# Kernel tuning notes

Hardware: AMD Instinct MI355X
Metric: run time of the kernel (lower is better)

The kernel has to match this reference:

```python
import jax, jax.numpy as jnp
import numpy as np

DIM = 384
HEADS = 6
K = 3  # kernel_size, stride = 1


def setup_inputs() -> dict:
    key = jax.random.key(0)
    ks = jax.random.split(key, 7)
    B, H, W, C = 16, 56, 56, DIM
    sc = 1.0 / np.sqrt(C)
    return {
        "x_map": jax.random.normal(ks[0], (B, H, W, C), dtype=jnp.float32),
        # Linear weights stored [in, out] (torch stores [out, in]; math identical)
        "W_attn": jax.random.normal(ks[1], (C, HEADS * K * K), dtype=jnp.float32) * sc,
        "b_attn": jax.random.normal(ks[2], (HEADS * K * K,), dtype=jnp.float32) * 0.02,
        "W_v": jax.random.normal(ks[3], (C, C), dtype=jnp.float32) * sc,
        "b_v": jax.random.normal(ks[4], (C,), dtype=jnp.float32) * 0.02,
        "W_proj": jax.random.normal(ks[5], (C, C), dtype=jnp.float32) * sc,
        "b_proj": jax.random.normal(ks[6], (C,), dtype=jnp.float32) * 0.02,
    }


def reference(x_map, W_attn, b_attn, W_v, b_v, W_proj, b_proj):
    B, H, W, C = x_map.shape
    k, heads = K, HEADS
    hd = C // heads
    pad = k // 2

    # attention logits per output pixel: [B, H*W, heads, k*k], softmax over window
    a = x_map @ W_attn + b_attn                     # [B,H,W,heads*k*k]
    a = jax.nn.softmax(a.reshape(B, H * W, heads, k * k), axis=-1)

    v = x_map @ W_v + b_v                           # [B,H,W,C]
    vp = jnp.pad(v, ((0, 0), (pad, pad), (pad, pad), (0, 0)))
    # k*k shifted views == F.unfold with row-major (ki,kj) kernel order
    patches = jnp.stack(
        [vp[:, i:i + H, j:j + W, :] for i in range(k) for j in range(k)],
        axis=3,
    )                                               # [B,H,W,k*k,C]
    patches = patches.reshape(B, H * W, k * k, heads, hd)

    # softmax-weighted sum over the k*k window, per head
    y = jnp.einsum('bpKhd,bphK->bphd', patches, a)  # [B,H*W,heads,hd]
    y = y.reshape(B, H, W, C)
    return y @ W_proj + b_proj
```

## Files before the change

kernel.cpp:

```cpp
#include <hip/hip_runtime.h>
#include <math.h>

#define NPIX 50176
#define CDIM 384
#define HEADS 6
#define NLOGIT 54
#define HH 56
#define WW 56
#define NCAT 448
#define KSTEPS 12
#define NCH_V 28
#define NCH_P 24

typedef __attribute__((ext_vector_type(8))) __bf16 bf16x8;
typedef __attribute__((ext_vector_type(4))) float f32x4;

__device__ __forceinline__ void glds16(const void* g, void* l) {
  __builtin_amdgcn_global_load_lds(
      (const __attribute__((address_space(1))) unsigned int*)g,
      (__attribute__((address_space(3))) unsigned int*)l, 16, 0, 0);
}

__global__ __launch_bounds__(256) void prep_kernel(
    const float* __restrict__ W_v, const float* __restrict__ W_proj,
    const float* __restrict__ W_attn, const float* __restrict__ b_attn,
    __bf16* __restrict__ Wcat_frag, __bf16* __restrict__ Wtp_frag,
    float* __restrict__ bpad) {
  const int gid = blockIdx.x * 256 + threadIdx.x;
  const int NV = KSTEPS * NCH_V * 64;
  const int NP = KSTEPS * NCH_P * 64;
  if (gid < NV) {
    const int ks   = gid / (NCH_V * 64);
    const int rem  = gid % (NCH_V * 64);
    const int ni   = rem >> 6;
    const int lane = rem & 63;
    const int n  = ni * 16 + (lane & 15);
    const int kb = ks * 32 + (lane >> 4) * 8;
    bf16x8 o;
    #pragma unroll
    for (int q = 0; q < 8; ++q) {
      const int k = kb + q;
      float val;
      if (n < CDIM) val = W_v[k * CDIM + n];
      else {
        const int nn = n - CDIM;
        val = (nn < NLOGIT) ? W_attn[k * NLOGIT + nn] : 0.f;
      }
      o[q] = (__bf16)val;
    }
    *(bf16x8*)&Wcat_frag[(size_t)gid * 8] = o;
  } else if (gid < NV + NP) {
    const int r    = gid - NV;
    const int ks   = r / (NCH_P * 64);
    const int rem  = r % (NCH_P * 64);
    const int ni   = rem >> 6;
    const int lane = rem & 63;
    const int n  = ni * 16 + (lane & 15);
    const int kb = ks * 32 + (lane >> 4) * 8;
    bf16x8 o;
    #pragma unroll
    for (int q = 0; q < 8; ++q) o[q] = (__bf16)W_proj[(kb + q) * CDIM + n];
    *(bf16x8*)&Wtp_frag[(size_t)r * 8] = o;
  } else if (gid < NV + NP + 64) {
    const int n = gid - NV - NP;
    bpad[n] = (n < NLOGIT) ? b_attn[n] : 0.f;
  }
}

__global__ __launch_bounds__(256) void gemm_v_logit_kernel(
    const float* __restrict__ X, const __bf16* __restrict__ Wcat_frag,
    const float* __restrict__ b_v, __bf16* __restrict__ v,
    const float* __restrict__ bpad, float* __restrict__ attn) {
  __shared__ char smem[NCH_V * 1024];
  __bf16* Bs = (__bf16*)smem;
  float (*Ls)[68] = (float(*)[68])smem;

  const int tid  = threadIdx.x;
  const int wave = tid >> 6;
  const int lane = tid & 63;
  const int bm   = blockIdx.x * 64;
  const int frow = lane & 15;
  const int fk8  = (lane >> 4) * 8;

  const int arow = bm + wave * 16 + frow;
  const float* xrow = X + (size_t)arow * CDIM + fk8;

  f32x4 acc[28] = {};
  float4 pa0 = *(const float4*)(xrow + 0);
  float4 pa1 = *(const float4*)(xrow + 4);

  for (int ks = 0; ks < KSTEPS; ++ks) {
    #pragma unroll
    for (int c = 0; c < 7; ++c) {
      const int chunk = wave * 7 + c;
      glds16(Wcat_frag + ((size_t)(ks * NCH_V + chunk) * 64 + lane) * 8,
             Bs + chunk * 512);
    }
    bf16x8 a;
    a[0] = (__bf16)pa0.x; a[1] = (__bf16)pa0.y; a[2] = (__bf16)pa0.z; a[3] = (__bf16)pa0.w;
    a[4] = (__bf16)pa1.x; a[5] = (__bf16)pa1.y; a[6] = (__bf16)pa1.z; a[7] = (__bf16)pa1.w;
    if (ks < KSTEPS - 1) {
      pa0 = *(const float4*)(xrow + (ks + 1) * 32 + 0);
      pa1 = *(const float4*)(xrow + (ks + 1) * 32 + 4);
    }
    __syncthreads();

    #pragma unroll
    for (int ni = 0; ni < 28; ++ni) {
      const bf16x8 b = *(const bf16x8*)&Bs[(ni * 64 + lane) * 8];
      acc[ni] = __builtin_amdgcn_mfma_f32_16x16x32_bf16(a, b, acc[ni], 0, 0, 0);
    }
    __syncthreads();
  }

  const int orow = (lane >> 4) * 4;

  #pragma unroll
  for (int ni = 0; ni < 24; ++ni) {
    const int n = ni * 16 + frow;
    const float bvl = b_v[n];
    #pragma unroll
    for (int r = 0; r < 4; ++r) {
      const int m = bm + wave * 16 + orow + r;
      v[(size_t)m * CDIM + n] = (__bf16)(acc[ni][r] + bvl);
    }
  }

  float bvl[4];
  #pragma unroll
  for (int ni = 0; ni < 4; ++ni) bvl[ni] = bpad[ni * 16 + frow];
  #pragma unroll
  for (int ni = 0; ni < 4; ++ni)
    #pragma unroll
    for (int r = 0; r < 4; ++r)
      Ls[wave * 16 + orow + r][ni * 16 + frow] = acc[24 + ni][r] + bvl[ni];
  __syncthreads();

  #pragma unroll
  for (int it = 0; it < 2; ++it) {
    const int task = it * 256 + tid;
    if (task < 64 * HEADS) {
      const int pl = task / HEADS;
      const int h  = task % HEADS;
      const float* row = &Ls[pl][h * 9];
      float m = row[0];
      #pragma unroll
      for (int w = 1; w < 9; ++w) m = fmaxf(m, row[w]);
      float e[9], s = 0.f;
      #pragma unroll
      for (int w = 0; w < 9; ++w) { e[w] = __expf(row[w] - m); s += e[w]; }
      const float inv = 1.f / s;
      float* op = &attn[(size_t)(bm + pl) * NLOGIT + h * 9];
      #pragma unroll
      for (int w = 0; w < 9; ++w) op[w] = e[w] * inv;
    }
  }
}

__global__ __launch_bounds__(256) void gemm_proj_kernel(
    const __bf16* __restrict__ Y, const __bf16* __restrict__ Wtp_frag,
    const float* __restrict__ bias, float* __restrict__ Out) {
  __shared__ __bf16 Bs[NCH_P * 512];

  const int tid  = threadIdx.x;
  const int wave = tid >> 6;
  const int lane = tid & 63;
  const int bm   = blockIdx.x * 64;
  const int frow = lane & 15;
  const int fk8  = (lane >> 4) * 8;

  const int arow = bm + wave * 16 + frow;
  const __bf16* yrow = Y + (size_t)arow * CDIM + fk8;

  f32x4 acc[24] = {};
  bf16x8 a = *(const bf16x8*)(yrow);

  for (int ks = 0; ks < KSTEPS; ++ks) {
    #pragma unroll
    for (int c = 0; c < 6; ++c) {
      const int chunk = wave * 6 + c;
      glds16(Wtp_frag + ((size_t)(ks * NCH_P + chunk) * 64 + lane) * 8,
             Bs + chunk * 512);
    }
    bf16x8 a_next;
    if (ks < KSTEPS - 1) a_next = *(const bf16x8*)(yrow + (ks + 1) * 32);
    __syncthreads();

    #pragma unroll
    for (int ni = 0; ni < 24; ++ni) {
      const bf16x8 b = *(const bf16x8*)&Bs[(ni * 64 + lane) * 8];
      acc[ni] = __builtin_amdgcn_mfma_f32_16x16x32_bf16(a, b, acc[ni], 0, 0, 0);
    }
    __syncthreads();
    a = a_next;
  }

  const int orow = (lane >> 4) * 4;
  #pragma unroll
  for (int ni = 0; ni < 24; ++ni) {
    const int n = ni * 16 + frow;
    const float bvl = bias[n];
    #pragma unroll
    for (int r = 0; r < 4; ++r) {
      const int m = bm + wave * 16 + orow + r;
      Out[(size_t)m * CDIM + n] = acc[ni][r] + bvl;
    }
  }
}

__global__ __launch_bounds__(256) void aggregate_kernel(
    const __bf16* __restrict__ v, const float* __restrict__ attn,
    __bf16* __restrict__ y) {
  const int idx = blockIdx.x * 256 + threadIdx.x;
  const int cg = idx % 48;
  const int pg = idx / 48;
  const int c  = cg * 8;
  const int b  = pg / ((HH / 4) * WW);
  const int r2 = pg % ((HH / 4) * WW);
  const int i0 = (r2 / WW) * 4;
  const int j  = r2 % WW;
  const int head = c >> 6;

  const int pbase = (b * HH + i0) * WW + j;
  float aw[4][9];
  #pragma unroll
  for (int p = 0; p < 4; ++p) {
    const float* ap = attn + (size_t)(pbase + p * WW) * NLOGIT + head * 9;
    #pragma unroll
    for (int w = 0; w < 9; ++w) aw[p][w] = ap[w];
  }

  const bool j0ok = (j > 0), j2ok = (j < WW - 1);
  float acc[4][8] = {};

  #pragma unroll
  for (int li = 0; li < 6; ++li) {
    const int ii = i0 - 1 + li;
    if (ii < 0 || ii >= HH) continue;
    const __bf16* vrow = v + ((size_t)(b * HH + ii) * WW + j) * CDIM + c;
    float ch[3][8];
    #pragma unroll
    for (int kj = 0; kj < 3; ++kj) {
      const bool ok = (kj == 0) ? j0ok : (kj == 2) ? j2ok : true;
      if (ok) {
        const bf16x8 vv = *(const bf16x8*)(vrow + (kj - 1) * CDIM);
        #pragma unroll
        for (int q = 0; q < 8; ++q) ch[kj][q] = (float)vv[q];
      } else {
        #pragma unroll
        for (int q = 0; q < 8; ++q) ch[kj][q] = 0.f;
      }
    }
    #pragma unroll
    for (int p = 0; p < 4; ++p) {
      const int ki = li - p;
      if (ki < 0 || ki > 2) continue;
      #pragma unroll
      for (int kj = 0; kj < 3; ++kj) {
        const float w = aw[p][ki * 3 + kj];
        #pragma unroll
        for (int q = 0; q < 8; ++q) acc[p][q] += w * ch[kj][q];
      }
    }
  }

  #pragma unroll
  for (int p = 0; p < 4; ++p) {
    bf16x8 o;
    #pragma unroll
    for (int q = 0; q < 8; ++q) o[q] = (__bf16)acc[p][q];
    *(bf16x8*)&y[(size_t)(pbase + p * WW) * CDIM + c] = o;
  }
}

extern "C" void kernel_launch(void* const* d_in, const int* in_sizes, int n_in,
                              void* d_out, int out_size, void* d_ws,
                              size_t ws_size, hipStream_t stream) {
  const float* x      = (const float*)d_in[0];
  const float* W_attn = (const float*)d_in[1];
  const float* b_attn = (const float*)d_in[2];
  const float* W_v    = (const float*)d_in[3];
  const float* b_v    = (const float*)d_in[4];
  const float* W_proj = (const float*)d_in[5];
  const float* b_proj = (const float*)d_in[6];
  float* out = (float*)d_out;

  char* w = (char*)d_ws;
  __bf16* v    = (__bf16*)w;  w += (size_t)NPIX * CDIM * 2;
  __bf16* y    = (__bf16*)w;  w += (size_t)NPIX * CDIM * 2;
  float*  attn = (float*)w;   w += (size_t)NPIX * NLOGIT * 4;
  __bf16* Wcat_frag = (__bf16*)w;  w += (size_t)NCAT * CDIM * 2;
  __bf16* Wtp_frag  = (__bf16*)w;  w += (size_t)CDIM * CDIM * 2;
  float*  bpad = (float*)w;   w += 64 * 4;

  const int prep_n = KSTEPS * NCH_V * 64 + KSTEPS * NCH_P * 64 + 64;
  prep_kernel<<<(prep_n + 255) / 256, 256, 0, stream>>>(
      W_v, W_proj, W_attn, b_attn, Wcat_frag, Wtp_frag, bpad);

  gemm_v_logit_kernel<<<NPIX / 64, 256, 0, stream>>>(
      x, Wcat_frag, b_v, v, bpad, attn);

  aggregate_kernel<<<(NPIX / 4 * 48) / 256, 256, 0, stream>>>(v, attn, y);

  gemm_proj_kernel<<<NPIX / 64, 256, 0, stream>>>(y, Wtp_frag, b_proj, out);
}
```

Measured before the change: 118.1 us.

## Split GEMM N dimension across two blocks and double-buffer weight tiles in LDS

Both GEMM kernels now launch a 2D grid that splits the output columns in half. Each block holds half the accumulators (14 or 12 fragments instead of 28 or 24), which lowers register pressure and doubles the block count. Weight tiles are double-buffered in LDS: the next K-step is prefetched while the current one runs, so one barrier per step replaces two. The cost is that each A row is now read and converted by both N-halves, doubling X traffic, and the softmax epilogue runs only in the by==1 blocks, which creates load imbalance.

```diff
diff --git a/kernel.cpp b/kernel.cpp
--- a/kernel.cpp
+++ b/kernel.cpp
@@ -71,88 +71,110 @@
     const float* __restrict__ X, const __bf16* __restrict__ Wcat_frag,
     const float* __restrict__ b_v, __bf16* __restrict__ v,
     const float* __restrict__ bpad, float* __restrict__ attn) {
-  __shared__ char smem[NCH_V * 1024];
-  __bf16* Bs = (__bf16*)smem;
+  __shared__ char smem[2 * 14 * 1024];
   float (*Ls)[68] = (float(*)[68])smem;
 
   const int tid  = threadIdx.x;
   const int wave = tid >> 6;
   const int lane = tid & 63;
   const int bm   = blockIdx.x * 64;
+  const int by   = blockIdx.y;
+  const int nbase = by * 14;
   const int frow = lane & 15;
   const int fk8  = (lane >> 4) * 8;
 
   const int arow = bm + wave * 16 + frow;
   const float* xrow = X + (size_t)arow * CDIM + fk8;
 
-  f32x4 acc[28] = {};
+  f32x4 acc[14] = {};
+
+  #pragma unroll
+  for (int c = 0; c < 4; ++c) {
+    const int chunk = wave * 4 + c;
+    if (chunk < 14)
+      glds16(Wcat_frag + ((size_t)(0 * NCH_V + nbase + chunk) * 64 + lane) * 8,
+             (__bf16*)smem + chunk * 512);
+  }
   float4 pa0 = *(const float4*)(xrow + 0);
   float4 pa1 = *(const float4*)(xrow + 4);
-
+  __syncthreads();
+
+  int buf = 0;
   for (int ks = 0; ks < KSTEPS; ++ks) {
-    #pragma unroll
-    for (int c = 0; c < 7; ++c) {
-      const int chunk = wave * 7 + c;
-      glds16(Wcat_frag + ((size_t)(ks * NCH_V + chunk) * 64 + lane) * 8,
-             Bs + chunk * 512);
+    if (ks + 1 < KSTEPS) {
+      __bf16* dst = (__bf16*)smem + (buf ^ 1) * 14 * 512;
+      #pragma unroll
+      for (int c = 0; c < 4; ++c) {
+        const int chunk = wave * 4 + c;
+        if (chunk < 14)
+          glds16(Wcat_frag +
+                     ((size_t)((ks + 1) * NCH_V + nbase + chunk) * 64 + lane) * 8,
+                 dst + chunk * 512);
+      }
     }
     bf16x8 a;
     a[0] = (__bf16)pa0.x; a[1] = (__bf16)pa0.y; a[2] = (__bf16)pa0.z; a[3] = (__bf16)pa0.w;
     a[4] = (__bf16)pa1.x; a[5] = (__bf16)pa1.y; a[6] = (__bf16)pa1.z; a[7] = (__bf16)pa1.w;
-    if (ks < KSTEPS - 1) {
+    if (ks + 1 < KSTEPS) {
       pa0 = *(const float4*)(xrow + (ks + 1) * 32 + 0);
       pa1 = *(const float4*)(xrow + (ks + 1) * 32 + 4);
     }
+
+    const __bf16* Bc = (const __bf16*)smem + buf * 14 * 512;
+    #pragma unroll
+    for (int ni = 0; ni < 14; ++ni) {
+      const bf16x8 b = *(const bf16x8*)&Bc[(ni * 64 + lane) * 8];
+      acc[ni] = __builtin_amdgcn_mfma_f32_16x16x32_bf16(a, b, acc[ni], 0, 0, 0);
+    }
     __syncthreads();
-
-    #pragma unroll
-    for (int ni = 0; ni < 28; ++ni) {
-      const bf16x8 b = *(const bf16x8*)&Bs[(ni * 64 + lane) * 8];
-      acc[ni] = __builtin_amdgcn_mfma_f32_16x16x32_bf16(a, b, acc[ni], 0, 0, 0);
-    }
+    buf ^= 1;
+  }
+
+  const int orow = (lane >> 4) * 4;
+  const int nv = (by == 0) ? 14 : 10;
+
+  #pragma unroll
+  for (int ni = 0; ni < 14; ++ni) {
+    if (ni < nv) {
+      const int n = by * 224 + ni * 16 + frow;
+      const float bvl = b_v[n];
+      #pragma unroll
+      for (int r = 0; r < 4; ++r) {
+        const int m = bm + wave * 16 + orow + r;
+        v[(size_t)m * CDIM + n] = (__bf16)(acc[ni][r] + bvl);
+      }
+    }
+  }
+
+  if (by == 1) {
+    float bvl[4];
+    #pragma unroll
+    for (int ni = 0; ni < 4; ++ni) bvl[ni] = bpad[ni * 16 + frow];
+    #pragma unroll
+    for (int ni = 0; ni < 4; ++ni)
+      #pragma unroll
+      for (int r = 0; r < 4; ++r)
+        Ls[wave * 16 + orow + r][ni * 16 + frow] = acc[10 + ni][r] + bvl[ni];
     __syncthreads();
-  }
-
-  const int orow = (lane >> 4) * 4;
-
-  #pragma unroll
-  for (int ni = 0; ni < 24; ++ni) {
-    const int n = ni * 16 + frow;
-    const float bvl = b_v[n];
-    #pragma unroll
-    for (int r = 0; r < 4; ++r) {
-      const int m = bm + wave * 16 + orow + r;
-      v[(size_t)m * CDIM + n] = (__bf16)(acc[ni][r] + bvl);
-    }
-  }
-
-  float bvl[4];
-  #pragma unroll
-  for (int ni = 0; ni < 4; ++ni) bvl[ni] = bpad[ni * 16 + frow];
-  #pragma unroll
-  for (int ni = 0; ni < 4; ++ni)
-    #pragma unroll
-    for (int r = 0; r < 4; ++r)
-      Ls[wave * 16 + orow + r][ni * 16 + frow] = acc[24 + ni][r] + bvl[ni];
-  __syncthreads();
-
-  #pragma unroll
-  for (int it = 0; it < 2; ++it) {
-    const int task = it * 256 + tid;
-    if (task < 64 * HEADS) {
-      const int pl = task / HEADS;
-      const int h  = task % HEADS;
-      const float* row = &Ls[pl][h * 9];
-      float m = row[0];
-      #pragma unroll
-      for (int w = 1; w < 9; ++w) m = fmaxf(m, row[w]);
-      float e[9], s = 0.f;
-      #pragma unroll
-      for (int w = 0; w < 9; ++w) { e[w] = __expf(row[w] - m); s += e[w]; }
-      const float inv = 1.f / s;
-      float* op = &attn[(size_t)(bm + pl) * NLOGIT + h * 9];
-      #pragma unroll
-      for (int w = 0; w < 9; ++w) op[w] = e[w] * inv;
+
+    #pragma unroll
+    for (int it = 0; it < 2; ++it) {
+      const int task = it * 256 + tid;
+      if (task < 64 * HEADS) {
+        const int pl = task / HEADS;
+        const int h  = task % HEADS;
+        const float* row = &Ls[pl][h * 9];
+        float m = row[0];
+        #pragma unroll
+        for (int w = 1; w < 9; ++w) m = fmaxf(m, row[w]);
+        float e[9], s = 0.f;
+        #pragma unroll
+        for (int w = 0; w < 9; ++w) { e[w] = __expf(row[w] - m); s += e[w]; }
+        const float inv = 1.f / s;
+        float* op = &attn[(size_t)(bm + pl) * NLOGIT + h * 9];
+        #pragma unroll
+        for (int w = 0; w < 9; ++w) op[w] = e[w] * inv;
+      }
     }
   }
 }
@@ -160,45 +182,61 @@
 __global__ __launch_bounds__(256) void gemm_proj_kernel(
     const __bf16* __restrict__ Y, const __bf16* __restrict__ Wtp_frag,
     const float* __restrict__ bias, float* __restrict__ Out) {
-  __shared__ __bf16 Bs[NCH_P * 512];
+  __shared__ __bf16 Bs[2 * 12 * 512];
 
   const int tid  = threadIdx.x;
   const int wave = tid >> 6;
   const int lane = tid & 63;
   const int bm   = blockIdx.x * 64;
+  const int by   = blockIdx.y;
+  const int nbase = by * 12;
   const int frow = lane & 15;
   const int fk8  = (lane >> 4) * 8;
 
   const int arow = bm + wave * 16 + frow;
   const __bf16* yrow = Y + (size_t)arow * CDIM + fk8;
 
-  f32x4 acc[24] = {};
+  f32x4 acc[12] = {};
+
+  #pragma unroll
+  for (int c = 0; c < 3; ++c) {
+    const int chunk = wave * 3 + c;
+    glds16(Wtp_frag + ((size_t)(nbase + chunk) * 64 + lane) * 8,
+           Bs + chunk * 512);
+  }
   bf16x8 a = *(const bf16x8*)(yrow);
-
+  __syncthreads();
+
+  int buf = 0;
   for (int ks = 0; ks < KSTEPS; ++ks) {
-    #pragma unroll
-    for (int c = 0; c < 6; ++c) {
-      const int chunk = wave * 6 + c;
-      glds16(Wtp_frag + ((size_t)(ks * NCH_P + chunk) * 64 + lane) * 8,
-             Bs + chunk * 512);
+    if (ks + 1 < KSTEPS) {
+      __bf16* dst = Bs + (buf ^ 1) * 12 * 512;
+      #pragma unroll
+      for (int c = 0; c < 3; ++c) {
+        const int chunk = wave * 3 + c;
+        glds16(Wtp_frag +
+                   ((size_t)((ks + 1) * NCH_P + nbase + chunk) * 64 + lane) * 8,
+               dst + chunk * 512);
+      }
     }
     bf16x8 a_next;
-    if (ks < KSTEPS - 1) a_next = *(const bf16x8*)(yrow + (ks + 1) * 32);
+    if (ks + 1 < KSTEPS) a_next = *(const bf16x8*)(yrow + (ks + 1) * 32);
+
+    const __bf16* Bc = Bs + buf * 12 * 512;
+    #pragma unroll
+    for (int ni = 0; ni < 12; ++ni) {
+      const bf16x8 b = *(const bf16x8*)&Bc[(ni * 64 + lane) * 8];
+      acc[ni] = __builtin_amdgcn_mfma_f32_16x16x32_bf16(a, b, acc[ni], 0, 0, 0);
+    }
     __syncthreads();
-
-    #pragma unroll
-    for (int ni = 0; ni < 24; ++ni) {
-      const bf16x8 b = *(const bf16x8*)&Bs[(ni * 64 + lane) * 8];
-      acc[ni] = __builtin_amdgcn_mfma_f32_16x16x32_bf16(a, b, acc[ni], 0, 0, 0);
-    }
-    __syncthreads();
+    buf ^= 1;
     a = a_next;
   }
 
   const int orow = (lane >> 4) * 4;
   #pragma unroll
-  for (int ni = 0; ni < 24; ++ni) {
-    const int n = ni * 16 + frow;
+  for (int ni = 0; ni < 12; ++ni) {
+    const int n = by * 192 + ni * 16 + frow;
     const float bvl = bias[n];
     #pragma unroll
     for (int r = 0; r < 4; ++r) {
@@ -297,10 +335,11 @@
   prep_kernel<<<(prep_n + 255) / 256, 256, 0, stream>>>(
       W_v, W_proj, W_attn, b_attn, Wcat_frag, Wtp_frag, bpad);
 
-  gemm_v_logit_kernel<<<NPIX / 64, 256, 0, stream>>>(
+  gemm_v_logit_kernel<<<dim3(NPIX / 64, 2), 256, 0, stream>>>(
       x, Wcat_frag, b_v, v, bpad, attn);
 
   aggregate_kernel<<<(NPIX / 4 * 48) / 256, 256, 0, stream>>>(v, attn, y);
 
-  gemm_proj_kernel<<<NPIX / 64, 256, 0, stream>>>(y, Wtp_frag, b_proj, out);
-}
+  gemm_proj_kernel<<<dim3(NPIX / 64, 2), 256, 0, stream>>>(
+      y, Wtp_frag, b_proj, out);
+}
```

New measurement: 109.0 us (median of 2 runs). -7.7%, faster.

## Pre-cast X to bf16, split GEMM N across blocks, double-buffer weight tiles

Applied to the files above, without the earlier changes.

Adds a separate kernel that converts X to bf16, so the first GEMM reads half the bytes for A. Both GEMMs now split the output columns over a second grid dimension, which gives smaller accumulator arrays and twice as many blocks. Weight fragments are double-buffered in LDS so the next k-step's load overlaps the MFMAs, leaving one barrier per step instead of two. In exchange it adds an extra full read and write pass over X and an extra launch, and each block re-reads its A rows twice.

```diff
diff --git a/kernel.cpp b/kernel.cpp
--- a/kernel.cpp
+++ b/kernel.cpp
@@ -7,7 +7,6 @@
 #define NLOGIT 54
 #define HH 56
 #define WW 56
-#define NCAT 448
 #define KSTEPS 12
 #define NCH_V 28
 #define NCH_P 24
@@ -67,145 +66,150 @@
   }
 }
 
+__global__ __launch_bounds__(256) void cast_x_kernel(
+    const float* __restrict__ x, __bf16* __restrict__ xb) {
+  const size_t i = (size_t)blockIdx.x * 256 + threadIdx.x;
+  const float4* src = (const float4*)x + i * 4;
+  const float4 f0 = src[0];
+  const float4 f1 = src[1];
+  const float4 f2 = src[2];
+  const float4 f3 = src[3];
+  bf16x8 o0, o1;
+  o0[0] = (__bf16)f0.x; o0[1] = (__bf16)f0.y; o0[2] = (__bf16)f0.z; o0[3] = (__bf16)f0.w;
+  o0[4] = (__bf16)f1.x; o0[5] = (__bf16)f1.y; o0[6] = (__bf16)f1.z; o0[7] = (__bf16)f1.w;
+  o1[0] = (__bf16)f2.x; o1[1] = (__bf16)f2.y; o1[2] = (__bf16)f2.z; o1[3] = (__bf16)f2.w;
+  o1[4] = (__bf16)f3.x; o1[5] = (__bf16)f3.y; o1[6] = (__bf16)f3.z; o1[7] = (__bf16)f3.w;
+  ((bf16x8*)xb)[i * 2]     = o0;
+  ((bf16x8*)xb)[i * 2 + 1] = o1;
+}
+
+template <int NCH, int STRIDE, int NBASE, bool LOGIT, bool F32OUT>
+__device__ __forceinline__ void gemm_body(
+    const __bf16* __restrict__ A, const __bf16* __restrict__ Wf,
+    const float* __restrict__ bias, void* __restrict__ out,
+    const float* __restrict__ bpad, float* __restrict__ attn,
+    __bf16* Bs, int bm, int tid) {
+  constexpr int CPW = NCH / 4;
+  const int wave = tid >> 6;
+  const int lane = tid & 63;
+  const int frow = lane & 15;
+  const int fk8  = (lane >> 4) * 8;
+  const int arow = bm + wave * 16 + frow;
+  const __bf16* xrow = A + (size_t)arow * CDIM + fk8;
+
+  f32x4 acc[NCH] = {};
+
+  #pragma unroll
+  for (int c = 0; c < CPW; ++c) {
+    const int chunk = wave * CPW + c;
+    glds16(Wf + ((size_t)(NBASE + chunk) * 64 + lane) * 8, Bs + chunk * 512);
+  }
+  bf16x8 a = *(const bf16x8*)xrow;
+  __syncthreads();
+
+  int buf = 0;
+  for (int ks = 0; ks < KSTEPS; ++ks) {
+    if (ks + 1 < KSTEPS) {
+      __bf16* dst = Bs + (buf ^ 1) * NCH * 512;
+      #pragma unroll
+      for (int c = 0; c < CPW; ++c) {
+        const int chunk = wave * CPW + c;
+        glds16(Wf + ((size_t)((ks + 1) * STRIDE + NBASE + chunk) * 64 + lane) * 8,
+               dst + chunk * 512);
+      }
+    }
+    bf16x8 a_next;
+    if (ks + 1 < KSTEPS) a_next = *(const bf16x8*)(xrow + (ks + 1) * 32);
+
+    const __bf16* Bc = Bs + buf * NCH * 512;
+    #pragma unroll
+    for (int ni = 0; ni < NCH; ++ni) {
+      const bf16x8 b = *(const bf16x8*)&Bc[(ni * 64 + lane) * 8];
+      acc[ni] = __builtin_amdgcn_mfma_f32_16x16x32_bf16(a, b, acc[ni], 0, 0, 0);
+    }
+    __syncthreads();
+    buf ^= 1;
+    a = a_next;
+  }
+
+  const int orow = (lane >> 4) * 4;
+  constexpr int NV = LOGIT ? NCH - 4 : NCH;
+
+  #pragma unroll
+  for (int ni = 0; ni < NV; ++ni) {
+    const int n = (NBASE + ni) * 16 + frow;
+    const float bvl = bias[n];
+    #pragma unroll
+    for (int r = 0; r < 4; ++r) {
+      const int m = bm + wave * 16 + orow + r;
+      const float val = acc[ni][r] + bvl;
+      if constexpr (F32OUT)
+        ((float*)out)[(size_t)m * CDIM + n] = val;
+      else
+        ((__bf16*)out)[(size_t)m * CDIM + n] = (__bf16)val;
+    }
+  }
+
+  if constexpr (LOGIT) {
+    float (*Ls)[68] = (float(*)[68])Bs;
+    __syncthreads();
+    float bvl[4];
+    #pragma unroll
+    for (int ni = 0; ni < 4; ++ni) bvl[ni] = bpad[ni * 16 + frow];
+    #pragma unroll
+    for (int ni = 0; ni < 4; ++ni)
+      #pragma unroll
+      for (int r = 0; r < 4; ++r)
+        Ls[wave * 16 + orow + r][ni * 16 + frow] = acc[NV + ni][r] + bvl[ni];
+    __syncthreads();
+
+    #pragma unroll
+    for (int it = 0; it < 2; ++it) {
+      const int task = it * 256 + tid;
+      if (task < 64 * HEADS) {
+        const int pl = task / HEADS;
+        const int h  = task % HEADS;
+        const float* row = &Ls[pl][h * 9];
+        float m = row[0];
+        #pragma unroll
+        for (int w = 1; w < 9; ++w) m = fmaxf(m, row[w]);
+        float e[9], s = 0.f;
+        #pragma unroll
+        for (int w = 0; w < 9; ++w) { e[w] = __expf(row[w] - m); s += e[w]; }
+        const float inv = 1.f / s;
+        float* op = &attn[(size_t)(bm + pl) * NLOGIT + h * 9];
+        #pragma unroll
+        for (int w = 0; w < 9; ++w) op[w] = e[w] * inv;
+      }
+    }
+  }
+}
+
 __global__ __launch_bounds__(256) void gemm_v_logit_kernel(
-    const float* __restrict__ X, const __bf16* __restrict__ Wcat_frag,
+    const __bf16* __restrict__ xb, const __bf16* __restrict__ Wcat_frag,
     const float* __restrict__ b_v, __bf16* __restrict__ v,
     const float* __restrict__ bpad, float* __restrict__ attn) {
-  __shared__ char smem[NCH_V * 1024];
-  __bf16* Bs = (__bf16*)smem;
-  float (*Ls)[68] = (float(*)[68])smem;
-
-  const int tid  = threadIdx.x;
-  const int wave = tid >> 6;
-  const int lane = tid & 63;
-  const int bm   = blockIdx.x * 64;
-  const int frow = lane & 15;
-  const int fk8  = (lane >> 4) * 8;
-
-  const int arow = bm + wave * 16 + frow;
-  const float* xrow = X + (size_t)arow * CDIM + fk8;
-
-  f32x4 acc[28] = {};
-  float4 pa0 = *(const float4*)(xrow + 0);
-  float4 pa1 = *(const float4*)(xrow + 4);
-
-  for (int ks = 0; ks < KSTEPS; ++ks) {
-    #pragma unroll
-    for (int c = 0; c < 7; ++c) {
-      const int chunk = wave * 7 + c;
-      glds16(Wcat_frag + ((size_t)(ks * NCH_V + chunk) * 64 + lane) * 8,
-             Bs + chunk * 512);
-    }
-    bf16x8 a;
-    a[0] = (__bf16)pa0.x; a[1] = (__bf16)pa0.y; a[2] = (__bf16)pa0.z; a[3] = (__bf16)pa0.w;
-    a[4] = (__bf16)pa1.x; a[5] = (__bf16)pa1.y; a[6] = (__bf16)pa1.z; a[7] = (__bf16)pa1.w;
-    if (ks < KSTEPS - 1) {
-      pa0 = *(const float4*)(xrow + (ks + 1) * 32 + 0);
-      pa1 = *(const float4*)(xrow + (ks + 1) * 32 + 4);
-    }
-    __syncthreads();
-
-    #pragma unroll
-    for (int ni = 0; ni < 28; ++ni) {
-      const bf16x8 b = *(const bf16x8*)&Bs[(ni * 64 + lane) * 8];
-      acc[ni] = __builtin_amdgcn_mfma_f32_16x16x32_bf16(a, b, acc[ni], 0, 0, 0);
-    }
-    __syncthreads();
-  }
-
-  const int orow = (lane >> 4) * 4;
-
-  #pragma unroll
-  for (int ni = 0; ni < 24; ++ni) {
-    const int n = ni * 16 + frow;
-    const float bvl = b_v[n];
-    #pragma unroll
-    for (int r = 0; r < 4; ++r) {
-      const int m = bm + wave * 16 + orow + r;
-      v[(size_t)m * CDIM + n] = (__bf16)(acc[ni][r] + bvl);
-    }
-  }
-
-  float bvl[4];
-  #pragma unroll
-  for (int ni = 0; ni < 4; ++ni) bvl[ni] = bpad[ni * 16 + frow];
-  #pragma unroll
-  for (int ni = 0; ni < 4; ++ni)
-    #pragma unroll
-    for (int r = 0; r < 4; ++r)
-      Ls[wave * 16 + orow + r][ni * 16 + frow] = acc[24 + ni][r] + bvl[ni];
-  __syncthreads();
-
-  #pragma unroll
-  for (int it = 0; it < 2; ++it) {
-    const int task = it * 256 + tid;
-    if (task < 64 * HEADS) {
-      const int pl = task / HEADS;
-      const int h  = task % HEADS;
-      const float* row = &Ls[pl][h * 9];
-      float m = row[0];
-      #pragma unroll
-      for (int w = 1; w < 9; ++w) m = fmaxf(m, row[w]);
-      float e[9], s = 0.f;
-      #pragma unroll
-      for (int w = 0; w < 9; ++w) { e[w] = __expf(row[w] - m); s += e[w]; }
-      const float inv = 1.f / s;
-      float* op = &attn[(size_t)(bm + pl) * NLOGIT + h * 9];
-      #pragma unroll
-      for (int w = 0; w < 9; ++w) op[w] = e[w] * inv;
-    }
-  }
+  __shared__ __bf16 Bs[2 * 16 * 512];
+  const int bm = blockIdx.x * 64;
+  if (blockIdx.y == 0)
+    gemm_body<16, NCH_V, 0, false, false>(
+        xb, Wcat_frag, b_v, v, bpad, attn, Bs, bm, threadIdx.x);
+  else
+    gemm_body<12, NCH_V, 16, true, false>(
+        xb, Wcat_frag, b_v, v, bpad, attn, Bs, bm, threadIdx.x);
 }
 
 __global__ __launch_bounds__(256) void gemm_proj_kernel(
     const __bf16* __restrict__ Y, const __bf16* __restrict__ Wtp_frag,
     const float* __restrict__ bias, float* __restrict__ Out) {
-  __shared__ __bf16 Bs[NCH_P * 512];
-
-  const int tid  = threadIdx.x;
-  const int wave = tid >> 6;
-  const int lane = tid & 63;
-  const int bm   = blockIdx.x * 64;
-  const int frow = lane & 15;
-  const int fk8  = (lane >> 4) * 8;
-
-  const int arow = bm + wave * 16 + frow;
-  const __bf16* yrow = Y + (size_t)arow * CDIM + fk8;
-
-  f32x4 acc[24] = {};
-  bf16x8 a = *(const bf16x8*)(yrow);
-
-  for (int ks = 0; ks < KSTEPS; ++ks) {
-    #pragma unroll
-    for (int c = 0; c < 6; ++c) {
-      const int chunk = wave * 6 + c;
-      glds16(Wtp_frag + ((size_t)(ks * NCH_P + chunk) * 64 + lane) * 8,
-             Bs + chunk * 512);
-    }
-    bf16x8 a_next;
-    if (ks < KSTEPS - 1) a_next = *(const bf16x8*)(yrow + (ks + 1) * 32);
-    __syncthreads();
-
-    #pragma unroll
-    for (int ni = 0; ni < 24; ++ni) {
-      const bf16x8 b = *(const bf16x8*)&Bs[(ni * 64 + lane) * 8];
-      acc[ni] = __builtin_amdgcn_mfma_f32_16x16x32_bf16(a, b, acc[ni], 0, 0, 0);
-    }
-    __syncthreads();
-    a = a_next;
-  }
-
-  const int orow = (lane >> 4) * 4;
-  #pragma unroll
-  for (int ni = 0; ni < 24; ++ni) {
-    const int n = ni * 16 + frow;
-    const float bvl = bias[n];
-    #pragma unroll
-    for (int r = 0; r < 4; ++r) {
-      const int m = bm + wave * 16 + orow + r;
-      Out[(size_t)m * CDIM + n] = acc[ni][r] + bvl;
-    }
-  }
+  __shared__ __bf16 Bs[2 * 12 * 512];
+  const int bm = blockIdx.x * 64;
+  if (blockIdx.y == 0)
+    gemm_body<12, NCH_P, 0, false, true>(
+        Y, Wtp_frag, bias, Out, nullptr, nullptr, Bs, bm, threadIdx.x);
+  else
+    gemm_body<12, NCH_P, 12, false, true>(
+        Y, Wtp_frag, bias, Out, nullptr, nullptr, Bs, bm, threadIdx.x);
 }
 
 __global__ __launch_bounds__(256) void aggregate_kernel(
@@ -286,10 +290,11 @@
   float* out = (float*)d_out;
 
   char* w = (char*)d_ws;
+  __bf16* xb   = (__bf16*)w;  w += (size_t)NPIX * CDIM * 2;
   __bf16* v    = (__bf16*)w;  w += (size_t)NPIX * CDIM * 2;
   __bf16* y    = (__bf16*)w;  w += (size_t)NPIX * CDIM * 2;
   float*  attn = (float*)w;   w += (size_t)NPIX * NLOGIT * 4;
-  __bf16* Wcat_frag = (__bf16*)w;  w += (size_t)NCAT * CDIM * 2;
+  __bf16* Wcat_frag = (__bf16*)w;  w += (size_t)(NCH_V * 16) * CDIM * 2;
   __bf16* Wtp_frag  = (__bf16*)w;  w += (size_t)CDIM * CDIM * 2;
   float*  bpad = (float*)w;   w += 64 * 4;
 
@@ -297,10 +302,13 @@
   prep_kernel<<<(prep_n + 255) / 256, 256, 0, stream>>>(
       W_v, W_proj, W_attn, b_attn, Wcat_frag, Wtp_frag, bpad);
 
-  gemm_v_logit_kernel<<<NPIX / 64, 256, 0, stream>>>(
-      x, Wcat_frag, b_v, v, bpad, attn);
+  cast_x_kernel<<<(NPIX * CDIM / 16) / 256, 256, 0, stream>>>(x, xb);
+
+  gemm_v_logit_kernel<<<dim3(NPIX / 64, 2), 256, 0, stream>>>(
+      xb, Wcat_frag, b_v, v, bpad, attn);
 
   aggregate_kernel<<<(NPIX / 4 * 48) / 256, 256, 0, stream>>>(v, attn, y);
 
-  gemm_proj_kernel<<<NPIX / 64, 256, 0, stream>>>(y, Wtp_frag, b_proj, out);
-}
+  gemm_proj_kernel<<<dim3(NPIX / 64, 2), 256, 0, stream>>>(
+      y, Wtp_frag, b_proj, out);
+}
```

Result: slower. 123.1 us (+4.2%).
